# Kernel optimization log

Measured on AMD Instinct MI355X. Metric: run time of the kernel, lower is better.

Reference implementation:

```python
import jax, jax.numpy as jnp
import numpy as np

B, N, K, HID, L, OUT, HEADS = 2, 512, 30, 128, 3, 400, 4
FF = 4 * HID


def gather_nodes(nodes, idx):
    # nodes [B,N,C], idx [B,N,K] -> [B,N,K,C]
    return jax.vmap(lambda n, i: n[i])(nodes, idx)


def cat_edge_endpoints(h_E, h_V, E_idx):
    # h_i uses E_idx[:,:,0] (self node) broadcast over K, h_j gathers neighbors
    idx_i = jnp.broadcast_to(E_idx[:, :, :1], E_idx.shape)
    h_i = gather_nodes(h_V, idx_i)
    h_j = gather_nodes(h_V, E_idx)
    return jnp.concatenate([h_i, h_j, h_E], axis=-1)  # [B,N,K,3*HID]


def norm(x, g, b, eps=1e-6):
    # Ingraham-style Normalize: unbiased var, eps added to sigma too
    mu = x.mean(-1, keepdims=True)
    sigma = jnp.sqrt(x.var(-1, keepdims=True, ddof=1) + eps)
    return g * (x - mu) / (sigma + eps) + b


def edge_attention(h_E, h_EV, wq, wk, wv, wo, mask_attend):
    b, n, k, H = h_E.shape
    d = H // HEADS
    Q = (h_E @ wq).reshape(b, n, k, HEADS, d).transpose(0, 1, 3, 2, 4)   # [B,N,h,K,d]
    Kk = (h_EV @ wk).reshape(b, n, k, HEADS, d).transpose(0, 1, 3, 2, 4)
    Vv = (h_EV @ wv).reshape(b, n, k, HEADS, d).transpose(0, 1, 3, 2, 4)
    logits = jnp.einsum('bnhqd,bnhkd->bnhqk', Q, Kk) / np.float32(np.sqrt(d))
    m = mask_attend[:, :, None, :, None]                 # [B,N,1,K,1]
    mask = m * jnp.swapaxes(m, -1, -2)                   # [B,N,1,K,K]
    logits = jnp.where(mask > 0, logits, jnp.finfo(jnp.float32).min)
    attend = jax.nn.softmax(logits, axis=-1) * mask
    upd = jnp.einsum('bnhqk,bnhkd->bnhqd', attend, Vv)
    upd = upd.transpose(0, 1, 3, 2, 4).reshape(b, n, k, H)
    return upd @ wo


def merge_duplicate_edges(hE, E_idx):
    # scatter edges into dense [B,N,N,H], transpose, gather reverse edge, average
    b, n, k, h = hE.shape
    bi = jnp.arange(b)[:, None, None]
    ni = jnp.arange(n)[None, :, None]
    coll = jnp.zeros((b, n, n, h), hE.dtype).at[bi, ni, E_idx].set(hE)
    rev = coll.transpose(0, 2, 1, 3)[bi, ni, E_idx]
    return (hE + rev) / 2


def setup_inputs() -> dict:
    key = jax.random.key(0)
    ks = iter(jax.random.split(key, 32))

    def xav(k, shape):
        fan_in, fan_out = shape[-2], shape[-1]
        return jax.random.normal(k, shape, jnp.float32) * np.float32(np.sqrt(2.0 / (fan_in + fan_out)))

    V = jax.random.normal(next(ks), (B, N, HID), jnp.float32)
    E = jax.random.normal(next(ks), (B, N, K, HID), jnp.float32)
    x_mask = jnp.ones((B, N), jnp.float32)
    E_idx = jax.random.randint(next(ks), (B, N, K), 0, N)
    # slot 0 is the self edge, as in k-NN graphs
    E_idx = E_idx.at[:, :, 0].set(jnp.arange(N)[None, :])
    inp = dict(V=V, E=E, x_mask=x_mask, E_idx=E_idx)
    inp['Wv_w'] = xav(next(ks), (HID, HID)); inp['Wv_b'] = jnp.zeros((HID,), jnp.float32)
    inp['We_w'] = xav(next(ks), (HID, HID)); inp['We_b'] = jnp.zeros((HID,), jnp.float32)
    inp['WQ'] = xav(next(ks), (L, HID, HID))
    inp['WK'] = xav(next(ks), (L, 3 * HID, HID))
    inp['WV'] = xav(next(ks), (L, 3 * HID, HID))
    inp['WO'] = xav(next(ks), (L, HID, HID))
    inp['ln1_g'] = jnp.ones((L, HID), jnp.float32); inp['ln1_b'] = jnp.zeros((L, HID), jnp.float32)
    inp['ln2_g'] = jnp.ones((L, HID), jnp.float32); inp['ln2_b'] = jnp.zeros((L, HID), jnp.float32)
    inp['ff1_w'] = xav(next(ks), (L, HID, FF)); inp['ff1_b'] = jnp.zeros((L, FF), jnp.float32)
    inp['ff2_w'] = xav(next(ks), (L, FF, HID)); inp['ff2_b'] = jnp.zeros((L, HID), jnp.float32)
    inp['Wout_w'] = xav(next(ks), (HID, OUT)); inp['Wout_b'] = jnp.zeros((OUT,), jnp.float32)
    return inp


def reference(V, E, x_mask, E_idx, Wv_w, Wv_b, We_w, We_b, WQ, WK, WV, WO,
              ln1_g, ln1_b, ln2_g, ln2_b, ff1_w, ff1_b, ff2_w, ff2_b,
              Wout_w, Wout_b):
    h_V = V @ Wv_w + Wv_b                                   # [B,N,HID]
    h_E = E @ We_w + We_b                                   # [B,N,K,HID]
    mask_attend = gather_nodes(x_mask[..., None], E_idx)[..., 0] * x_mask[..., None]
    for l in range(L):
        h_EV = cat_edge_endpoints(h_E, h_V, E_idx)          # [B,N,K,3*HID]
        dh = edge_attention(h_E, h_EV, WQ[l], WK[l], WV[l], WO[l], mask_attend)
        h_E = norm(h_E + dh, ln1_g[l], ln1_b[l])
        dh = jnp.maximum(h_E @ ff1_w[l] + ff1_b[l], 0.0) @ ff2_w[l] + ff2_b[l]
        h_E = norm(h_E + dh, ln2_g[l], ln2_b[l])
        h_E = h_E * x_mask[:, :, None, None]                # mask_E
    h_out = h_E @ Wout_w + Wout_b                           # [B,N,K,OUT]
    return merge_duplicate_edges(h_out, E_idx)
```

## Files before the change

### kernel.cpp

```cpp
#include <hip/hip_runtime.h>

#define NB 512
#define KNB 30
#define HID 128
#define NL 3
#define NOUT 400
#define NFF 512

typedef _Float16 f16;
typedef _Float16 f16x8 __attribute__((ext_vector_type(8)));
typedef _Float16 f16x4 __attribute__((ext_vector_type(4)));
typedef float f32x4 __attribute__((ext_vector_type(4)));

#define MFMA16(a, b, c) __builtin_amdgcn_mfma_f32_16x16x32_f16(a, b, c, 0, 0, 0)

#define PK_WE   0
#define PK_WQ   16384
#define PK_WK   65536
#define PK_WV   114688
#define PK_WO   163840
#define PK_F1   212992
#define PK_F2   409600
#define PK_WOUT 606208
#define PK_TOTAL 657408

__global__ void k_hv(const float* __restrict__ V, const float* __restrict__ Wv,
                     const float* __restrict__ bv, float* __restrict__ hV) {
  int idx = blockIdx.x * 256 + threadIdx.x;
  int row = idx >> 7, c = idx & 127;
  const float* vr = V + row * HID;
  float acc = bv[c];
  for (int i = 0; i < HID; ++i) acc = fmaf(vr[i], Wv[i * HID + c], acc);
  hV[idx] = acc;
}

__global__ void k_tables(const float* __restrict__ hV, const float* __restrict__ WK,
                         const float* __restrict__ WVp, float* __restrict__ tbl) {
  int idx = blockIdx.x * 256 + threadIdx.x;
  int c = idx & 127;
  int row = (idx >> 7) & 1023;
  int t = idx >> 17;
  int l = t >> 2, part = t & 3;
  const float* W;
  if (part == 0)      W = WK  + l * 3 * HID * HID;
  else if (part == 1) W = WK  + l * 3 * HID * HID + HID * HID;
  else if (part == 2) W = WVp + l * 3 * HID * HID;
  else                W = WVp + l * 3 * HID * HID + HID * HID;
  const float* hr = hV + row * HID;
  float acc = 0.f;
  for (int i = 0; i < HID; ++i) acc = fmaf(hr[i], W[i * HID + c], acc);
  tbl[idx] = acc;
}

__device__ __forceinline__ void pack_one(const float* W, int N, int r, f16* dst) {
  int j = r & 7, l = (r >> 3) & 63, t = r >> 9;
  int NT = N >> 4;
  int nt = t % NT, ks = t / NT;
  int k = ks * 32 + ((l >> 4) << 3) + j;
  int c = nt * 16 + (l & 15);
  dst[r] = (f16)W[k * N + c];
}

__global__ void k_pack(const float* __restrict__ We, const float* __restrict__ WQ,
                       const float* __restrict__ WK, const float* __restrict__ WV,
                       const float* __restrict__ WO, const float* __restrict__ f1w,
                       const float* __restrict__ f2w, const float* __restrict__ Wout,
                       f16* __restrict__ P) {
  int idx = blockIdx.x * 256 + threadIdx.x;
  if (idx >= PK_TOTAL) return;
  const float* W; int N; int r; f16* dst;
  if (idx < 212992) {
    int s = idx >> 14; r = idx & 16383; N = 128;
    dst = P + (idx - r);
    if (s == 0) W = We;
    else if (s < 4) W = WQ + (s - 1) * 16384;
    else if (s < 7) W = WK + (s - 4) * 49152 + 32768;
    else if (s < 10) W = WV + (s - 7) * 49152 + 32768;
    else W = WO + (s - 10) * 16384;
  } else if (idx < 409600) {
    int t = (idx - 212992) >> 16; r = (idx - 212992) & 65535;
    W = f1w + t * 65536; N = 512; dst = P + 212992 + t * 65536;
  } else if (idx < 606208) {
    int t = (idx - 409600) >> 16; r = (idx - 409600) & 65535;
    W = f2w + t * 65536; N = 128; dst = P + 409600 + t * 65536;
  } else {
    r = idx - 606208; W = Wout; N = 400; dst = P + 606208;
  }
  pack_one(W, N, r, dst);
}

__device__ __forceinline__ void mfma_block8(const f16* Ab, int astr, const f16x8* B,
                                            int nt0, int nt1, f32x4 acc[2][2],
                                            int ln, int g, int lane) {
  f16x8 af[2][4];
#pragma unroll
  for (int mt = 0; mt < 2; ++mt)
#pragma unroll
    for (int ks = 0; ks < 4; ++ks)
      af[mt][ks] = *(const f16x8*)&Ab[(mt * 16 + ln) * astr + ks * 32 + g * 8];
#pragma unroll
  for (int ks = 0; ks < 4; ++ks) {
    f16x8 b0 = B[(ks * 8 + nt0) * 64 + lane];
    f16x8 b1 = B[(ks * 8 + nt1) * 64 + lane];
#pragma unroll
    for (int mt = 0; mt < 2; ++mt) {
      acc[mt][0] = MFMA16(af[mt][ks], b0, acc[mt][0]);
      acc[mt][1] = MFMA16(af[mt][ks], b1, acc[mt][1]);
    }
  }
}

__device__ __forceinline__ void layer_norm_cvt(float (*hEp)[132], f16* hEhp,
                                               const float* __restrict__ gg,
                                               const float* __restrict__ bb,
                                               float mmul, int tid) {
  int r = tid >> 3, g8 = tid & 7;
  if (r < KNB) {
    float x[16]; float s1 = 0.f, s2 = 0.f;
    int cb = g8 * 16;
#pragma unroll
    for (int m = 0; m < 16; ++m) { x[m] = hEp[r][cb + m]; s1 += x[m]; s2 += x[m] * x[m]; }
#pragma unroll
    for (int o = 1; o < 8; o <<= 1) { s1 += __shfl_xor(s1, o); s2 += __shfl_xor(s2, o); }
    float mu = s1 * (1.f / 128.f);
    float var = fmaf(-s1, mu, s2) * (1.f / 127.f);
    float inv = 1.f / (sqrtf(var + 1e-6f) + 1e-6f);
    f16x8 h0, h1;
#pragma unroll
    for (int m = 0; m < 16; ++m) {
      int c = cb + m;
      float y = (gg[c] * (x[m] - mu) * inv + bb[c]) * mmul;
      hEp[r][c] = y;
      if (m < 8) h0[m] = (f16)y; else h1[m - 8] = (f16)y;
    }
    *(f16x8*)&hEhp[r * 136 + cb] = h0;
    *(f16x8*)&hEhp[r * 136 + cb + 8] = h1;
  }
}

__launch_bounds__(256, 2)
__global__ void k_main(
    const float* __restrict__ E, const int* __restrict__ Eix, const float* __restrict__ xm,
    const float* __restrict__ be,
    const float* __restrict__ l1g, const float* __restrict__ l1b,
    const float* __restrict__ l2g, const float* __restrict__ l2b,
    const float* __restrict__ f1b, const float* __restrict__ f2b,
    const float* __restrict__ bout,
    const f16* __restrict__ P, const float* __restrict__ tbl,
    float* __restrict__ gOUT) {
  __shared__ __align__(16) char SM[63744];
  float (*hE)[132] = (float(*)[132])SM;
  f16* hEh = (f16*)(SM + 16896);
  char* poolB = SM + 25600;
  f16* Qh   = (f16*)(poolB);
  f16* Kh   = (f16*)(poolB + 8704);
  f16* Vt   = (f16*)(poolB + 17408);
  f16* atth = (f16*)(poolB + 27648);
  f16* hidh = (f16*)(poolB);
  float* ma = (float*)(SM + 63488);
  int* eidx = (int*)(SM + 63616);

  const int tid = threadIdx.x;
  const int bid = blockIdx.x;
  const int b = bid >> 9, n = bid & (NB - 1);
  const int lane = tid & 63, wv = tid >> 6;
  const int ln = lane & 15, g = lane >> 4;

  {
    float4 z = make_float4(0.f, 0.f, 0.f, 0.f);
    float4* p = (float4*)(SM + 16896);
    for (int x = tid; x < 2912; x += 256) p[x] = z;
  }
  if (tid < 32) {
    int e = (tid < KNB) ? Eix[(b * NB + n) * KNB + tid] : 0;
    eidx[tid] = e;
    float mr = xm[b * NB + n];
    ma[tid] = (tid < KNB) ? mr * xm[b * NB + e] : 0.f;
  }
  __syncthreads();
  {
    const float4* Eg = (const float4*)(E + (size_t)(b * NB + n) * KNB * HID);
    for (int x = tid; x < 960; x += 256) {
      float4 e4 = Eg[x];
      int r = x >> 5, c = (x & 31) << 2;
      f16x4 h; h[0] = (f16)e4.x; h[1] = (f16)e4.y; h[2] = (f16)e4.z; h[3] = (f16)e4.w;
      *(f16x4*)&hEh[r * 136 + c] = h;
    }
  }
  const float mrow = xm[b * NB + n];
  __syncthreads();

  {
    f32x4 acc[2][2] = {};
    mfma_block8(hEh, 136, (const f16x8*)(P + PK_WE), wv, wv + 4, acc, ln, g, lane);
    __syncthreads();
#pragma unroll
    for (int nts = 0; nts < 2; ++nts) {
      int c = (wv + nts * 4) * 16 + ln;
      float bev = be[c];
#pragma unroll
      for (int mt = 0; mt < 2; ++mt)
#pragma unroll
        for (int i = 0; i < 4; ++i) {
          int r = mt * 16 + 4 * g + i;
          if (r < KNB) {
            float v = acc[mt][nts][i] + bev;
            hE[r][c] = v;
            hEh[r * 136 + c] = (f16)v;
          }
        }
    }
  }
  __syncthreads();

  for (int l = 0; l < NL; ++l) {
    const f16x8* PQ = (const f16x8*)(P + PK_WQ + l * 16384);
    const f16x8* PKk = (const f16x8*)(P + PK_WK + l * 16384);
    const f16x8* PV = (const f16x8*)(P + PK_WV + l * 16384);
    const f16x8* PO = (const f16x8*)(P + PK_WO + l * 16384);
    const f16x8* P1 = (const f16x8*)(P + PK_F1 + l * 65536);
    const f16x8* P2 = (const f16x8*)(P + PK_F2 + l * 65536);
    const float* Ki = tbl + (size_t)(l * 4 + 0) * (2 * NB * HID) + (size_t)b * NB * HID;
    const float* Kj = tbl + (size_t)(l * 4 + 1) * (2 * NB * HID) + (size_t)b * NB * HID;
    const float* Vi = tbl + (size_t)(l * 4 + 2) * (2 * NB * HID) + (size_t)b * NB * HID;
    const float* Vj = tbl + (size_t)(l * 4 + 3) * (2 * NB * HID) + (size_t)b * NB * HID;

    {
      int e0v = eidx[0];
      int er[2][4];
#pragma unroll
      for (int mt = 0; mt < 2; ++mt)
#pragma unroll
        for (int i = 0; i < 4; ++i) er[mt][i] = eidx[mt * 16 + 4 * g + i];
      float kib[2], vib[2], kjv[2][2][4], vjv[2][2][4];
#pragma unroll
      for (int nts = 0; nts < 2; ++nts) {
        int c = (wv + nts * 4) * 16 + ln;
        kib[nts] = Ki[e0v * 128 + c];
        vib[nts] = Vi[e0v * 128 + c];
#pragma unroll
        for (int mt = 0; mt < 2; ++mt)
#pragma unroll
          for (int i = 0; i < 4; ++i) {
            kjv[nts][mt][i] = Kj[er[mt][i] * 128 + c];
            vjv[nts][mt][i] = Vj[er[mt][i] * 128 + c];
          }
      }
      f32x4 qa[2][2] = {}, kk[2][2] = {}, va[2][2] = {};
      mfma_block8(hEh, 136, PQ, wv, wv + 4, qa, ln, g, lane);
      mfma_block8(hEh, 136, PKk, wv, wv + 4, kk, ln, g, lane);
      mfma_block8(hEh, 136, PV, wv, wv + 4, va, ln, g, lane);
#pragma unroll
      for (int nts = 0; nts < 2; ++nts) {
        int c = (wv + nts * 4) * 16 + ln;
#pragma unroll
        for (int mt = 0; mt < 2; ++mt)
#pragma unroll
          for (int i = 0; i < 4; ++i) {
            int r = mt * 16 + 4 * g + i;
            Qh[r * 136 + c] = (f16)qa[mt][nts][i];
            Kh[r * 136 + c] = (f16)(kk[mt][nts][i] + kib[nts] + kjv[nts][mt][i]);
            Vt[c * 40 + r]  = (f16)(va[mt][nts][i] + vib[nts] + vjv[nts][mt][i]);
          }
      }
    }
    __syncthreads();

    {
      int h = wv;
      f16* ath = atth + h * 1280;
      f16x8 qf[2], kf[2];
#pragma unroll
      for (int mt = 0; mt < 2; ++mt)
        qf[mt] = *(const f16x8*)&Qh[(mt * 16 + ln) * 136 + h * 32 + g * 8];
#pragma unroll
      for (int nt = 0; nt < 2; ++nt)
        kf[nt] = *(const f16x8*)&Kh[(nt * 16 + ln) * 136 + h * 32 + g * 8];
      f32x4 s[2][2] = {};
#pragma unroll
      for (int mt = 0; mt < 2; ++mt)
#pragma unroll
        for (int nt = 0; nt < 2; ++nt) s[mt][nt] = MFMA16(qf[mt], kf[nt], s[mt][nt]);
      float mk0 = ma[ln], mk1 = ma[16 + ln];
      const float scale = 0.17677669529663687f;
#pragma unroll
      for (int mt = 0; mt < 2; ++mt) {
#pragma unroll
        for (int i = 0; i < 4; ++i) {
          int q = mt * 16 + 4 * g + i;
          float mq = ma[q];
          float v0 = s[mt][0][i] * scale;
          float v1 = s[mt][1][i] * scale;
          v0 = (mq * mk0 > 0.f) ? v0 : -3.4028234663852886e38f;
          v1 = (mq * mk1 > 0.f) ? v1 : -3.4028234663852886e38f;
          float mx = fmaxf(v0, v1);
          mx = fmaxf(mx, __shfl_xor(mx, 1));
          mx = fmaxf(mx, __shfl_xor(mx, 2));
          mx = fmaxf(mx, __shfl_xor(mx, 4));
          mx = fmaxf(mx, __shfl_xor(mx, 8));
          float e0 = __expf(v0 - mx), e1 = __expf(v1 - mx);
          float sm = e0 + e1;
          sm += __shfl_xor(sm, 1); sm += __shfl_xor(sm, 2);
          sm += __shfl_xor(sm, 4); sm += __shfl_xor(sm, 8);
          float inv = 1.f / sm;
          ath[q * 40 + ln]      = (f16)(e0 * inv * (mq * mk0));
          ath[q * 40 + 16 + ln] = (f16)(e1 * inv * (mq * mk1));
        }
      }
      asm volatile("s_waitcnt lgkmcnt(0)" ::: "memory");
      __builtin_amdgcn_sched_barrier(0);
      f32x4 u[2][2] = {};
      f16x8 aat[2], vbf[2];
#pragma unroll
      for (int mt = 0; mt < 2; ++mt)
        aat[mt] = *(const f16x8*)&ath[(mt * 16 + ln) * 40 + g * 8];
#pragma unroll
      for (int nt = 0; nt < 2; ++nt)
        vbf[nt] = *(const f16x8*)&Vt[((2 * h + nt) * 16 + ln) * 40 + g * 8];
#pragma unroll
      for (int mt = 0; mt < 2; ++mt)
#pragma unroll
        for (int nt = 0; nt < 2; ++nt) u[mt][nt] = MFMA16(aat[mt], vbf[nt], u[mt][nt]);
#pragma unroll
      for (int mt = 0; mt < 2; ++mt)
#pragma unroll
        for (int nt = 0; nt < 2; ++nt)
#pragma unroll
          for (int i = 0; i < 4; ++i) {
            int r = mt * 16 + 4 * g + i;
            hEh[r * 136 + h * 32 + nt * 16 + ln] = (f16)u[mt][nt][i];
          }
    }
    __syncthreads();

    {
      f32x4 acc[2][2] = {};
      mfma_block8(hEh, 136, PO, wv, wv + 4, acc, ln, g, lane);
#pragma unroll
      for (int nts = 0; nts < 2; ++nts) {
        int c = (wv + nts * 4) * 16 + ln;
#pragma unroll
        for (int mt = 0; mt < 2; ++mt)
#pragma unroll
          for (int i = 0; i < 4; ++i) {
            int r = mt * 16 + 4 * g + i;
            if (r < KNB) hE[r][c] += acc[mt][nts][i];
          }
      }
    }
    __syncthreads();
    layer_norm_cvt(hE, hEh, l1g + l * HID, l1b + l * HID, 1.f, tid);
    __syncthreads();

    {
      f16x8 af[2][4];
#pragma unroll
      for (int mt = 0; mt < 2; ++mt)
#pragma unroll
        for (int ks = 0; ks < 4; ++ks)
          af[mt][ks] = *(const f16x8*)&hEh[(mt * 16 + ln) * 136 + ks * 32 + g * 8];
      f32x4 acc[2][8] = {};
#pragma unroll
      for (int ks = 0; ks < 4; ++ks)
#pragma unroll
        for (int t = 0; t < 8; ++t) {
          f16x8 bv = P1[(ks * 32 + wv + 4 * t) * 64 + lane];
          acc[0][t] = MFMA16(af[0][ks], bv, acc[0][t]);
          acc[1][t] = MFMA16(af[1][ks], bv, acc[1][t]);
        }
      const float* b1 = f1b + l * NFF;
#pragma unroll
      for (int t = 0; t < 8; ++t) {
        int c = (wv + 4 * t) * 16 + ln;
        float b1v = b1[c];
#pragma unroll
        for (int mt = 0; mt < 2; ++mt)
#pragma unroll
          for (int i = 0; i < 4; ++i) {
            int r = mt * 16 + 4 * g + i;
            hidh[r * 520 + c] = (f16)fmaxf(acc[mt][t][i] + b1v, 0.f);
          }
      }
    }
    __syncthreads();

    {
      f32x4 acc[2][2] = {};
#pragma unroll
      for (int ks = 0; ks < 16; ++ks) {
        f16x8 a0 = *(const f16x8*)&hidh[ln * 520 + ks * 32 + g * 8];
        f16x8 a1 = *(const f16x8*)&hidh[(16 + ln) * 520 + ks * 32 + g * 8];
        f16x8 b0 = P2[(ks * 8 + wv) * 64 + lane];
        f16x8 b1 = P2[(ks * 8 + wv + 4) * 64 + lane];
        acc[0][0] = MFMA16(a0, b0, acc[0][0]);
        acc[0][1] = MFMA16(a0, b1, acc[0][1]);
        acc[1][0] = MFMA16(a1, b0, acc[1][0]);
        acc[1][1] = MFMA16(a1, b1, acc[1][1]);
      }
      const float* b2 = f2b + l * HID;
#pragma unroll
      for (int nts = 0; nts < 2; ++nts) {
        int c = (wv + nts * 4) * 16 + ln;
        float b2v = b2[c];
#pragma unroll
        for (int mt = 0; mt < 2; ++mt)
#pragma unroll
          for (int i = 0; i < 4; ++i) {
            int r = mt * 16 + 4 * g + i;
            if (r < KNB) hE[r][c] += acc[mt][nts][i] + b2v;
          }
      }
    }
    __syncthreads();
    layer_norm_cvt(hE, hEh, l2g + l * HID, l2b + l * HID, mrow, tid);
    __syncthreads();
  }

  {
    float* gO = gOUT + (size_t)((b * NB + n) * KNB) * NOUT;
    f16x8 af[2][4];
#pragma unroll
    for (int mt = 0; mt < 2; ++mt)
#pragma unroll
      for (int ks = 0; ks < 4; ++ks)
        af[mt][ks] = *(const f16x8*)&hEh[(mt * 16 + ln) * 136 + ks * 32 + g * 8];
    const f16x8* PW = (const f16x8*)(P + PK_WOUT);
#pragma unroll
    for (int mt = 0; mt < 2; ++mt) {
      for (int nt = wv; nt < 25; nt += 4) {
        f32x4 acc = {};
#pragma unroll
        for (int ks = 0; ks < 4; ++ks) {
          f16x8 bv = PW[(ks * 25 + nt) * 64 + lane];
          acc = MFMA16(af[mt][ks], bv, acc);
        }
        int c = nt * 16 + ln;
        float bo = bout[c];
#pragma unroll
        for (int i = 0; i < 4; ++i) {
          int r = mt * 16 + 4 * g + i;
          if (r < KNB) gO[r * 400 + c] = acc[i] + bo;
        }
      }
    }
  }
}

__global__ void k_clearT(int* __restrict__ T) {
  int i = blockIdx.x * 256 + threadIdx.x;
  if (i < 2 * NB * NB) T[i] = 0;
}
__global__ void k_buildT(const int* __restrict__ Eix, int* __restrict__ T) {
  int idx = blockIdx.x * 256 + threadIdx.x;
  if (idx < 2 * NB * KNB) {
    int b = idx / (NB * KNB);
    int rem = idx % (NB * KNB);
    int i = rem / KNB, k = rem % KNB;
    int j = Eix[idx];
    atomicMax(&T[(b * NB + i) * NB + j], k + 1);
  }
}
__global__ void k_merge(const float* __restrict__ HO, const int* __restrict__ Eix,
                        const int* __restrict__ T, float* __restrict__ out) {
  int gid = blockIdx.x * 256 + threadIdx.x;
  if (gid >= 2 * NB * KNB * (NOUT / 4)) return;
  int c4 = gid % (NOUT / 4);
  int bnk = gid / (NOUT / 4);
  int b = bnk / (NB * KNB);
  int n = (bnk / KNB) % NB;
  int j = Eix[bnk];
  int kp = T[(b * NB + j) * NB + n];
  float4 a = ((const float4*)HO)[(size_t)bnk * (NOUT / 4) + c4];
  float4 rv = make_float4(0.f, 0.f, 0.f, 0.f);
  if (kp > 0) rv = ((const float4*)HO)[(size_t)((b * NB + j) * KNB + (kp - 1)) * (NOUT / 4) + c4];
  ((float4*)out)[gid] = make_float4(0.5f * (a.x + rv.x), 0.5f * (a.y + rv.y),
                                    0.5f * (a.z + rv.z), 0.5f * (a.w + rv.w));
}

extern "C" void kernel_launch(void* const* d_in, const int* in_sizes, int n_in,
                              void* d_out, int out_size, void* d_ws, size_t ws_size,
                              hipStream_t stream) {
  const float* V   = (const float*)d_in[0];
  const float* E   = (const float*)d_in[1];
  const float* xmk = (const float*)d_in[2];
  const int*   Eix = (const int*)d_in[3];
  const float* Wv  = (const float*)d_in[4];
  const float* bv  = (const float*)d_in[5];
  const float* We  = (const float*)d_in[6];
  const float* be  = (const float*)d_in[7];
  const float* WQ  = (const float*)d_in[8];
  const float* WK  = (const float*)d_in[9];
  const float* WVp = (const float*)d_in[10];
  const float* WO  = (const float*)d_in[11];
  const float* l1g = (const float*)d_in[12];
  const float* l1b = (const float*)d_in[13];
  const float* l2g = (const float*)d_in[14];
  const float* l2b = (const float*)d_in[15];
  const float* f1w = (const float*)d_in[16];
  const float* f1b = (const float*)d_in[17];
  const float* f2w = (const float*)d_in[18];
  const float* f2b = (const float*)d_in[19];
  const float* Wou = (const float*)d_in[20];
  const float* bou = (const float*)d_in[21];

  float* HO  = (float*)d_ws;
  float* tbl = HO + 12288000ull;
  float* hV  = tbl + 1572864ull;
  f16*   P   = (f16*)(hV + 131072ull);
  int*   T   = (int*)tbl;

  k_hv<<<512, 256, 0, stream>>>(V, Wv, bv, hV);
  k_tables<<<6144, 256, 0, stream>>>(hV, WK, WVp, tbl);
  k_pack<<<2568, 256, 0, stream>>>(We, WQ, WK, WVp, WO, f1w, f2w, Wou, P);
  k_main<<<1024, 256, 0, stream>>>(E, Eix, xmk, be, l1g, l1b, l2g, l2b,
                                   f1b, f2b, bou, P, tbl, HO);
  k_clearT<<<2048, 256, 0, stream>>>(T);
  k_buildT<<<120, 256, 0, stream>>>(Eix, T);
  k_merge<<<12000, 256, 0, stream>>>(HO, Eix, T, (float*)d_out);
}
```

Before: 342.7 us.

## Shrink k_main LDS via chunked FFN and reused attention buffers, fuse prep kernels

The FFN hidden layer is now computed in two 256-wide chunks, each immediately consumed by the second matmul, so the hidden buffer fits in the Q/K/V region. Attention probabilities are written over K after an extra barrier, which removes the separate attention buffer. Together these cut LDS from about 62KB to 52KB and raise launch bounds to 3 blocks per CU. The table, pack and clear kernels are merged into one launch and T is moved to its own region so buildT can run before k_main. The cost is extra barriers per layer and possible register pressure at the higher occupancy target.

```diff
diff --git a/kernel.cpp b/kernel.cpp
--- a/kernel.cpp
+++ b/kernel.cpp
@@ -13,6 +13,7 @@
 typedef float f32x4 __attribute__((ext_vector_type(4)));
 
 #define MFMA16(a, b, c) __builtin_amdgcn_mfma_f32_16x16x32_f16(a, b, c, 0, 0, 0)
+#define FLTMIN -3.4028234663852886e38f
 
 #define PK_WE   0
 #define PK_WQ   16384
@@ -34,24 +35,6 @@
   hV[idx] = acc;
 }
 
-__global__ void k_tables(const float* __restrict__ hV, const float* __restrict__ WK,
-                         const float* __restrict__ WVp, float* __restrict__ tbl) {
-  int idx = blockIdx.x * 256 + threadIdx.x;
-  int c = idx & 127;
-  int row = (idx >> 7) & 1023;
-  int t = idx >> 17;
-  int l = t >> 2, part = t & 3;
-  const float* W;
-  if (part == 0)      W = WK  + l * 3 * HID * HID;
-  else if (part == 1) W = WK  + l * 3 * HID * HID + HID * HID;
-  else if (part == 2) W = WVp + l * 3 * HID * HID;
-  else                W = WVp + l * 3 * HID * HID + HID * HID;
-  const float* hr = hV + row * HID;
-  float acc = 0.f;
-  for (int i = 0; i < HID; ++i) acc = fmaf(hr[i], W[i * HID + c], acc);
-  tbl[idx] = acc;
-}
-
 __device__ __forceinline__ void pack_one(const float* W, int N, int r, f16* dst) {
   int j = r & 7, l = (r >> 3) & 63, t = r >> 9;
   int NT = N >> 4;
@@ -61,32 +44,54 @@
   dst[r] = (f16)W[k * N + c];
 }
 
-__global__ void k_pack(const float* __restrict__ We, const float* __restrict__ WQ,
-                       const float* __restrict__ WK, const float* __restrict__ WV,
+__global__ void k_prep(const float* __restrict__ hV, const float* __restrict__ WK,
+                       const float* __restrict__ WVp, float* __restrict__ tbl,
+                       const float* __restrict__ We, const float* __restrict__ WQ,
                        const float* __restrict__ WO, const float* __restrict__ f1w,
                        const float* __restrict__ f2w, const float* __restrict__ Wout,
-                       f16* __restrict__ P) {
-  int idx = blockIdx.x * 256 + threadIdx.x;
-  if (idx >= PK_TOTAL) return;
-  const float* W; int N; int r; f16* dst;
-  if (idx < 212992) {
-    int s = idx >> 14; r = idx & 16383; N = 128;
-    dst = P + (idx - r);
-    if (s == 0) W = We;
-    else if (s < 4) W = WQ + (s - 1) * 16384;
-    else if (s < 7) W = WK + (s - 4) * 49152 + 32768;
-    else if (s < 10) W = WV + (s - 7) * 49152 + 32768;
-    else W = WO + (s - 10) * 16384;
-  } else if (idx < 409600) {
-    int t = (idx - 212992) >> 16; r = (idx - 212992) & 65535;
-    W = f1w + t * 65536; N = 512; dst = P + 212992 + t * 65536;
-  } else if (idx < 606208) {
-    int t = (idx - 409600) >> 16; r = (idx - 409600) & 65535;
-    W = f2w + t * 65536; N = 128; dst = P + 409600 + t * 65536;
+                       f16* __restrict__ P, int* __restrict__ T) {
+  int blk = blockIdx.x, tid = threadIdx.x;
+  if (blk < 6144) {
+    int idx = blk * 256 + tid;
+    int c = idx & 127;
+    int row = (idx >> 7) & 1023;
+    int t = idx >> 17;
+    int l = t >> 2, part = t & 3;
+    const float* W;
+    if (part == 0)      W = WK  + l * 3 * HID * HID;
+    else if (part == 1) W = WK  + l * 3 * HID * HID + HID * HID;
+    else if (part == 2) W = WVp + l * 3 * HID * HID;
+    else                W = WVp + l * 3 * HID * HID + HID * HID;
+    const float* hr = hV + row * HID;
+    float acc = 0.f;
+    for (int i = 0; i < HID; ++i) acc = fmaf(hr[i], W[i * HID + c], acc);
+    tbl[idx] = acc;
+  } else if (blk < 6144 + 2568) {
+    int idx = (blk - 6144) * 256 + tid;
+    if (idx >= PK_TOTAL) return;
+    const float* W; int N; int r; f16* dst;
+    if (idx < 212992) {
+      int s = idx >> 14; r = idx & 16383; N = 128;
+      dst = P + (idx - r);
+      if (s == 0) W = We;
+      else if (s < 4) W = WQ + (s - 1) * 16384;
+      else if (s < 7) W = WK + (s - 4) * 49152 + 32768;
+      else if (s < 10) W = WVp + (s - 7) * 49152 + 32768;
+      else W = WO + (s - 10) * 16384;
+    } else if (idx < 409600) {
+      int t = (idx - 212992) >> 16; r = (idx - 212992) & 65535;
+      W = f1w + t * 65536; N = 512; dst = P + 212992 + t * 65536;
+    } else if (idx < 606208) {
+      int t = (idx - 409600) >> 16; r = (idx - 409600) & 65535;
+      W = f2w + t * 65536; N = 128; dst = P + 409600 + t * 65536;
+    } else {
+      r = idx - 606208; W = Wout; N = 400; dst = P + 606208;
+    }
+    pack_one(W, N, r, dst);
   } else {
-    r = idx - 606208; W = Wout; N = 400; dst = P + 606208;
-  }
-  pack_one(W, N, r, dst);
+    int i = (blk - 8712) * 256 + tid;
+    if (i < 2 * NB * NB) T[i] = 0;
+  }
 }
 
 __device__ __forceinline__ void mfma_block8(const f16* Ab, int astr, const f16x8* B,
@@ -138,7 +143,7 @@
   }
 }
 
-__launch_bounds__(256, 2)
+__launch_bounds__(256, 3)
 __global__ void k_main(
     const float* __restrict__ E, const int* __restrict__ Eix, const float* __restrict__ xm,
     const float* __restrict__ be,
@@ -148,38 +153,36 @@
     const float* __restrict__ bout,
     const f16* __restrict__ P, const float* __restrict__ tbl,
     float* __restrict__ gOUT) {
-  __shared__ __align__(16) char SM[63744];
+  __shared__ __align__(16) char SM[53504];
   float (*hE)[132] = (float(*)[132])SM;
   f16* hEh = (f16*)(SM + 16896);
-  char* poolB = SM + 25600;
-  f16* Qh   = (f16*)(poolB);
-  f16* Kh   = (f16*)(poolB + 8704);
-  f16* Vt   = (f16*)(poolB + 17408);
-  f16* atth = (f16*)(poolB + 27648);
-  f16* hidh = (f16*)(poolB);
-  float* ma = (float*)(SM + 63488);
-  int* eidx = (int*)(SM + 63616);
+  f16* Qh  = (f16*)(SM + 25600);
+  f16* Kh  = (f16*)(SM + 34304);
+  f16* Vt  = (f16*)(SM + 43008);
+  float* ma = (float*)(SM + 53248);
+  int* eidx = (int*)(SM + 53376);
+  f16* hid = Qh;
 
   const int tid = threadIdx.x;
+  const int wv = tid >> 6, lane = tid & 63, ln = lane & 15, g = lane >> 4;
   const int bid = blockIdx.x;
   const int b = bid >> 9, n = bid & (NB - 1);
-  const int lane = tid & 63, wv = tid >> 6;
-  const int ln = lane & 15, g = lane >> 4;
+  const int ebase = (b * NB + n) * KNB;
 
   {
     float4 z = make_float4(0.f, 0.f, 0.f, 0.f);
     float4* p = (float4*)(SM + 16896);
-    for (int x = tid; x < 2912; x += 256) p[x] = z;
+    for (int x = tid; x < 2272; x += 256) p[x] = z;
   }
   if (tid < 32) {
-    int e = (tid < KNB) ? Eix[(b * NB + n) * KNB + tid] : 0;
+    int e = (tid < KNB) ? Eix[ebase + tid] : 0;
     eidx[tid] = e;
     float mr = xm[b * NB + n];
     ma[tid] = (tid < KNB) ? mr * xm[b * NB + e] : 0.f;
   }
   __syncthreads();
   {
-    const float4* Eg = (const float4*)(E + (size_t)(b * NB + n) * KNB * HID);
+    const float4* Eg = (const float4*)(E + (size_t)ebase * HID);
     for (int x = tid; x < 960; x += 256) {
       float4 e4 = Eg[x];
       int r = x >> 5, c = (x & 31) << 2;
@@ -267,69 +270,65 @@
     __syncthreads();
 
     {
-      int h = wv;
-      f16* ath = atth + h * 1280;
-      f16x8 qf[2], kf[2];
-#pragma unroll
-      for (int mt = 0; mt < 2; ++mt)
-        qf[mt] = *(const f16x8*)&Qh[(mt * 16 + ln) * 136 + h * 32 + g * 8];
+      const int h = wv;
+      const float scale = 0.17677669529663687f;
+      f16x8 aq[2], bk[2];
+#pragma unroll
+      for (int mt = 0; mt < 2; ++mt)
+        aq[mt] = *(const f16x8*)&Qh[(mt * 16 + ln) * 136 + h * 32 + g * 8];
 #pragma unroll
       for (int nt = 0; nt < 2; ++nt)
-        kf[nt] = *(const f16x8*)&Kh[(nt * 16 + ln) * 136 + h * 32 + g * 8];
+        bk[nt] = *(const f16x8*)&Kh[(nt * 16 + ln) * 136 + h * 32 + g * 8];
       f32x4 s[2][2] = {};
 #pragma unroll
       for (int mt = 0; mt < 2; ++mt)
 #pragma unroll
-        for (int nt = 0; nt < 2; ++nt) s[mt][nt] = MFMA16(qf[mt], kf[nt], s[mt][nt]);
+        for (int nt = 0; nt < 2; ++nt) s[mt][nt] = MFMA16(aq[mt], bk[nt], s[mt][nt]);
+      __syncthreads();
+      f16* Ph = Kh + h * 1024;
       float mk0 = ma[ln], mk1 = ma[16 + ln];
-      const float scale = 0.17677669529663687f;
 #pragma unroll
       for (int mt = 0; mt < 2; ++mt) {
 #pragma unroll
         for (int i = 0; i < 4; ++i) {
           int q = mt * 16 + 4 * g + i;
           float mq = ma[q];
-          float v0 = s[mt][0][i] * scale;
-          float v1 = s[mt][1][i] * scale;
-          v0 = (mq * mk0 > 0.f) ? v0 : -3.4028234663852886e38f;
-          v1 = (mq * mk1 > 0.f) ? v1 : -3.4028234663852886e38f;
+          float p0 = mq * mk0, p1 = mq * mk1;
+          float v0 = (p0 > 0.f) ? s[mt][0][i] * scale : FLTMIN;
+          float v1 = (p1 > 0.f) ? s[mt][1][i] * scale : FLTMIN;
           float mx = fmaxf(v0, v1);
           mx = fmaxf(mx, __shfl_xor(mx, 1));
           mx = fmaxf(mx, __shfl_xor(mx, 2));
           mx = fmaxf(mx, __shfl_xor(mx, 4));
           mx = fmaxf(mx, __shfl_xor(mx, 8));
-          float e0 = __expf(v0 - mx), e1 = __expf(v1 - mx);
-          float sm = e0 + e1;
+          float e0v = __expf(v0 - mx), e1v = __expf(v1 - mx);
+          float sm = e0v + e1v;
           sm += __shfl_xor(sm, 1); sm += __shfl_xor(sm, 2);
           sm += __shfl_xor(sm, 4); sm += __shfl_xor(sm, 8);
-          float inv = 1.f / sm;
-          ath[q * 40 + ln]      = (f16)(e0 * inv * (mq * mk0));
-          ath[q * 40 + 16 + ln] = (f16)(e1 * inv * (mq * mk1));
+          float iv = 1.f / sm;
+          Ph[q * 32 + ln]      = (f16)(e0v * iv * p0);
+          Ph[q * 32 + 16 + ln] = (f16)(e1v * iv * p1);
         }
       }
-      asm volatile("s_waitcnt lgkmcnt(0)" ::: "memory");
-      __builtin_amdgcn_sched_barrier(0);
+      f16x8 pa[2], vb[2];
+#pragma unroll
+      for (int mt = 0; mt < 2; ++mt)
+        pa[mt] = *(const f16x8*)&Ph[(mt * 16 + ln) * 32 + g * 8];
+#pragma unroll
+      for (int nt = 0; nt < 2; ++nt)
+        vb[nt] = *(const f16x8*)&Vt[((2 * h + nt) * 16 + ln) * 40 + g * 8];
       f32x4 u[2][2] = {};
-      f16x8 aat[2], vbf[2];
-#pragma unroll
-      for (int mt = 0; mt < 2; ++mt)
-        aat[mt] = *(const f16x8*)&ath[(mt * 16 + ln) * 40 + g * 8];
-#pragma unroll
-      for (int nt = 0; nt < 2; ++nt)
-        vbf[nt] = *(const f16x8*)&Vt[((2 * h + nt) * 16 + ln) * 40 + g * 8];
-#pragma unroll
-      for (int mt = 0; mt < 2; ++mt)
-#pragma unroll
-        for (int nt = 0; nt < 2; ++nt) u[mt][nt] = MFMA16(aat[mt], vbf[nt], u[mt][nt]);
+#pragma unroll
+      for (int mt = 0; mt < 2; ++mt)
+#pragma unroll
+        for (int nt = 0; nt < 2; ++nt) u[mt][nt] = MFMA16(pa[mt], vb[nt], u[mt][nt]);
 #pragma unroll
       for (int mt = 0; mt < 2; ++mt)
 #pragma unroll
         for (int nt = 0; nt < 2; ++nt)
 #pragma unroll
-          for (int i = 0; i < 4; ++i) {
-            int r = mt * 16 + 4 * g + i;
-            hEh[r * 136 + h * 32 + nt * 16 + ln] = (f16)u[mt][nt][i];
-          }
+          for (int i = 0; i < 4; ++i)
+            hEh[(mt * 16 + 4 * g + i) * 136 + h * 32 + nt * 16 + ln] = (f16)u[mt][nt][i];
     }
     __syncthreads();
 
@@ -353,49 +352,49 @@
     __syncthreads();
 
     {
-      f16x8 af[2][4];
+      f16x8 aff[2][4];
 #pragma unroll
       for (int mt = 0; mt < 2; ++mt)
 #pragma unroll
         for (int ks = 0; ks < 4; ++ks)
-          af[mt][ks] = *(const f16x8*)&hEh[(mt * 16 + ln) * 136 + ks * 32 + g * 8];
-      f32x4 acc[2][8] = {};
-#pragma unroll
-      for (int ks = 0; ks < 4; ++ks)
-#pragma unroll
-        for (int t = 0; t < 8; ++t) {
-          f16x8 bv = P1[(ks * 32 + wv + 4 * t) * 64 + lane];
-          acc[0][t] = MFMA16(af[0][ks], bv, acc[0][t]);
-          acc[1][t] = MFMA16(af[1][ks], bv, acc[1][t]);
+          aff[mt][ks] = *(const f16x8*)&hEh[(mt * 16 + ln) * 136 + ks * 32 + g * 8];
+      f32x4 ff[2][2] = {};
+      const float* b1 = f1b + l * NFF;
+#pragma unroll
+      for (int ch = 0; ch < 2; ++ch) {
+        f32x4 h1[2][4] = {};
+#pragma unroll
+        for (int ks = 0; ks < 4; ++ks)
+#pragma unroll
+          for (int t = 0; t < 4; ++t) {
+            f16x8 bv = P1[(ks * 32 + ch * 16 + t * 4 + wv) * 64 + lane];
+            h1[0][t] = MFMA16(aff[0][ks], bv, h1[0][t]);
+            h1[1][t] = MFMA16(aff[1][ks], bv, h1[1][t]);
+          }
+#pragma unroll
+        for (int t = 0; t < 4; ++t) {
+          int ntl = t * 4 + wv;
+          float b1v = b1[ch * 256 + ntl * 16 + ln];
+#pragma unroll
+          for (int mt = 0; mt < 2; ++mt)
+#pragma unroll
+            for (int i = 0; i < 4; ++i)
+              hid[(mt * 16 + 4 * g + i) * 264 + ntl * 16 + ln] =
+                  (f16)fmaxf(h1[mt][t][i] + b1v, 0.f);
         }
-      const float* b1 = f1b + l * NFF;
-#pragma unroll
-      for (int t = 0; t < 8; ++t) {
-        int c = (wv + 4 * t) * 16 + ln;
-        float b1v = b1[c];
-#pragma unroll
-        for (int mt = 0; mt < 2; ++mt)
-#pragma unroll
-          for (int i = 0; i < 4; ++i) {
-            int r = mt * 16 + 4 * g + i;
-            hidh[r * 520 + c] = (f16)fmaxf(acc[mt][t][i] + b1v, 0.f);
-          }
-      }
-    }
-    __syncthreads();
-
-    {
-      f32x4 acc[2][2] = {};
-#pragma unroll
-      for (int ks = 0; ks < 16; ++ks) {
-        f16x8 a0 = *(const f16x8*)&hidh[ln * 520 + ks * 32 + g * 8];
-        f16x8 a1 = *(const f16x8*)&hidh[(16 + ln) * 520 + ks * 32 + g * 8];
-        f16x8 b0 = P2[(ks * 8 + wv) * 64 + lane];
-        f16x8 b1 = P2[(ks * 8 + wv + 4) * 64 + lane];
-        acc[0][0] = MFMA16(a0, b0, acc[0][0]);
-        acc[0][1] = MFMA16(a0, b1, acc[0][1]);
-        acc[1][0] = MFMA16(a1, b0, acc[1][0]);
-        acc[1][1] = MFMA16(a1, b1, acc[1][1]);
+        __syncthreads();
+#pragma unroll
+        for (int k2 = 0; k2 < 8; ++k2) {
+          f16x8 a0 = *(const f16x8*)&hid[ln * 264 + k2 * 32 + g * 8];
+          f16x8 a1 = *(const f16x8*)&hid[(16 + ln) * 264 + k2 * 32 + g * 8];
+          f16x8 w0 = P2[((ch * 8 + k2) * 8 + wv) * 64 + lane];
+          f16x8 w1 = P2[((ch * 8 + k2) * 8 + wv + 4) * 64 + lane];
+          ff[0][0] = MFMA16(a0, w0, ff[0][0]);
+          ff[0][1] = MFMA16(a0, w1, ff[0][1]);
+          ff[1][0] = MFMA16(a1, w0, ff[1][0]);
+          ff[1][1] = MFMA16(a1, w1, ff[1][1]);
+        }
+        if (ch == 0) __syncthreads();
       }
       const float* b2 = f2b + l * HID;
 #pragma unroll
@@ -407,7 +406,7 @@
 #pragma unroll
           for (int i = 0; i < 4; ++i) {
             int r = mt * 16 + 4 * g + i;
-            if (r < KNB) hE[r][c] += acc[mt][nts][i] + b2v;
+            if (r < KNB) hE[r][c] += ff[mt][nts][i] + b2v;
           }
       }
     }
@@ -417,7 +416,7 @@
   }
 
   {
-    float* gO = gOUT + (size_t)((b * NB + n) * KNB) * NOUT;
+    float* gO = gOUT + (size_t)ebase * NOUT;
     f16x8 af[2][4];
 #pragma unroll
     for (int mt = 0; mt < 2; ++mt)
@@ -439,17 +438,13 @@
 #pragma unroll
         for (int i = 0; i < 4; ++i) {
           int r = mt * 16 + 4 * g + i;
-          if (r < KNB) gO[r * 400 + c] = acc[i] + bo;
+          if (r < KNB) gO[(size_t)r * NOUT + c] = acc[i] + bo;
         }
       }
     }
   }
 }
 
-__global__ void k_clearT(int* __restrict__ T) {
-  int i = blockIdx.x * 256 + threadIdx.x;
-  if (i < 2 * NB * NB) T[i] = 0;
-}
 __global__ void k_buildT(const int* __restrict__ Eix, int* __restrict__ T) {
   int idx = blockIdx.x * 256 + threadIdx.x;
   if (idx < 2 * NB * KNB) {
@@ -507,14 +502,12 @@
   float* tbl = HO + 12288000ull;
   float* hV  = tbl + 1572864ull;
   f16*   P   = (f16*)(hV + 131072ull);
-  int*   T   = (int*)tbl;
+  int*   T   = (int*)(P + PK_TOTAL + 256);
 
   k_hv<<<512, 256, 0, stream>>>(V, Wv, bv, hV);
-  k_tables<<<6144, 256, 0, stream>>>(hV, WK, WVp, tbl);
-  k_pack<<<2568, 256, 0, stream>>>(We, WQ, WK, WVp, WO, f1w, f2w, Wou, P);
+  k_prep<<<10760, 256, 0, stream>>>(hV, WK, WVp, tbl, We, WQ, WO, f1w, f2w, Wou, P, T);
+  k_buildT<<<120, 256, 0, stream>>>(Eix, T);
   k_main<<<1024, 256, 0, stream>>>(E, Eix, xmk, be, l1g, l1b, l2g, l2b,
                                    f1b, f2b, bou, P, tbl, HO);
-  k_clearT<<<2048, 256, 0, stream>>>(T);
-  k_buildT<<<120, 256, 0, stream>>>(Eix, T);
   k_merge<<<12000, 256, 0, stream>>>(HO, Eix, T, (float*)d_out);
 }
```

Measured after the change: 433.9 us. 1.27x slower.
